# Performance work log

Measured on AMD Instinct MI355X. Metric: run time of the kernel, lower is better.

The kernel has to match this reference:

```python
import jax, jax.numpy as jnp
import numpy as np

N_NODES = 100000
N_EDGES = 3200000
N_HID = 3
HEAD_OUT = 1024


def setup_inputs() -> dict:
    key = jax.random.key(0)
    ks = jax.random.split(key, 8)
    feat1 = jax.random.normal(ks[0], (N_NODES, 1), dtype=jnp.float32)
    feat2 = jax.random.normal(ks[1], (N_NODES, 1), dtype=jnp.float32)
    norm = jax.random.uniform(ks[2], (N_EDGES,), dtype=jnp.float32)
    src = jax.random.randint(ks[3], (N_EDGES,), 0, N_NODES, dtype=jnp.int32)
    dst = jax.random.randint(ks[4], (N_EDGES,), 0, N_NODES, dtype=jnp.int32)
    # per-layer GIN apply_func Linear(1,1): weight [n_hid,1,1], bias [n_hid,1]
    gin_w = jax.random.normal(ks[5], (N_HID, 1, 1), dtype=jnp.float32)
    gin_b = jax.random.normal(ks[6], (N_HID, 1), dtype=jnp.float32) * 0.1
    # head Linear(num_nodes, 1024), stored as [in, out]
    net_w = jax.random.normal(ks[7], (N_NODES, HEAD_OUT), dtype=jnp.float32) * (1.0 / np.sqrt(N_NODES))
    net_b = jnp.zeros((HEAD_OUT,), dtype=jnp.float32)
    return {"feat1": feat1, "feat2": feat2, "norm": norm, "src": src, "dst": dst,
            "gin_w": gin_w, "gin_b": gin_b, "net_w": net_w, "net_b": net_b}


def reference(feat1, feat2, norm, src, dst, gin_w, gin_b, net_w, net_b):
    n = feat1.shape[0]
    e_dtype = feat1.dtype
    # in-degree (same every layer); DGL mean over mailbox divides by in-degree
    deg = jax.ops.segment_sum(jnp.ones((src.shape[0],), e_dtype), dst, num_segments=n)
    inv_deg = (1.0 / jnp.maximum(deg, 1.0))[:, None]  # [N,1]

    def forward_each(feat):
        x = feat  # [N,1]
        saved = []
        for l in range(gin_w.shape[0]):
            msg = x[src] * norm[:, None]                                # gather + edge weight [E,1]
            agg = jax.ops.segment_sum(msg, dst, num_segments=n) * inv_deg  # mean aggregate [N,1]
            rst = (x + agg) @ gin_w[l].T + gin_b[l]                     # GIN: (1+eps)*x + agg, eps=0, then Linear
            saved.append(rst)                                           # forward hook captures pre-relu output
            x = jax.nn.relu(rst)
        feats = jnp.mean(jnp.stack(saved), axis=0)  # mean over layers [N,1]
        h = feats.reshape(1, -1)                    # flatten -> [1, N]
        return h @ net_w + net_b                    # [1, 1024]

    x1 = forward_each(feat1)
    x2 = forward_each(feat2)
    return jax.nn.sigmoid(jnp.sum(x1 * x2, axis=1, keepdims=True))  # [1,1]
```

## Files before the change

kernel.cpp:

```cpp
#include <hip/hip_runtime.h>
#include <math.h>

static constexpr int NN  = 100000;
static constexpr int NE  = 3200000;
static constexpr int HO  = 1024;
static constexpr int BSH = 5;
static constexpr int BMASK = 31;
static constexpr int NB  = 3125;
static constexpr int NBP = NB + 1;
static constexpr int PB  = 256;
static constexpr int AT  = 1024;
static constexpr int CHUNK = NE / PB;
static constexpr int PER_A = (NB + AT - 1) / AT;
static constexpr int RPB = 50;
static constexpr int HB  = NN / RPB;
static constexpr int CAP = 2048;
static constexpr int BT  = 49;
static constexpr int BSTRIDE = 1536;

typedef float f4v __attribute__((ext_vector_type(4)));

__device__ __forceinline__ int bucket_swz(int blk) {
    int x = blk & 7, g = blk >> 3;
    return (x < 5) ? x * 391 + g : 1955 + (x - 5) * 390 + g;
}

__global__ __launch_bounds__(AT) void partA_k(const float* __restrict__ f1,
                                              const float* __restrict__ f2,
                                              const int* __restrict__ src,
                                              const int* __restrict__ dst,
                                              const float* __restrict__ norm,
                                              int* __restrict__ loffg,
                                              uint2* __restrict__ blocked,
                                              float2* __restrict__ x0,
                                              float* __restrict__ xacc) {
    __shared__ int hist[NB];
    __shared__ int wt[16];
    int blk = blockIdx.x, t = threadIdx.x;
    int lane = t & 63, w = t >> 6;
    int gi = blk * AT + t;
    if (gi < NN) x0[gi] = make_float2(f1[gi], f2[gi]);
    if (blk == 0) {
        for (int i = t; i < 2 * HO; i += AT) xacc[i] = 0.f;
    }
    for (int i = t; i < NB; i += AT) hist[i] = 0;
    __syncthreads();
    int base = blk * CHUNK;
    for (int i = t; i < CHUNK; i += AT)
        atomicAdd(&hist[dst[base + i] >> BSH], 1);
    __syncthreads();
    int loc[PER_A]; int s = 0;
    int b0 = t * PER_A;
#pragma unroll
    for (int k = 0; k < PER_A; ++k) {
        int i = b0 + k;
        int v = (i < NB) ? hist[i] : 0;
        loc[k] = s; s += v;
    }
    int incl = s;
#pragma unroll
    for (int off = 1; off < 64; off <<= 1) {
        int v = __shfl_up(incl, off, 64);
        if (lane >= off) incl += v;
    }
    if (lane == 63) wt[w] = incl;
    __syncthreads();
    int wpre = 0;
#pragma unroll
    for (int k = 0; k < 16; ++k) if (k < w) wpre += wt[k];
    int carry = wpre + incl - s;
#pragma unroll
    for (int k = 0; k < PER_A; ++k) {
        int i = b0 + k;
        if (i < NB) {
            int e = carry + loc[k];
            loffg[blk * NBP + i] = e;
            hist[i] = e;
        }
    }
    __syncthreads();
    for (int i = t; i < CHUNK; i += AT) {
        int e = base + i;
        int d = dst[e];
        int pos = atomicAdd(&hist[d >> BSH], 1);
        blocked[base + pos] = make_uint2((unsigned)src[e] | ((unsigned)(d & BMASK) << 17),
                                         __float_as_uint(norm[e]));
    }
}

__global__ __launch_bounds__(256) void transT_k(const int* __restrict__ loffg,
                                                int* __restrict__ loffT) {
    __shared__ int tile[64][65];
    int bx = blockIdx.x % BT;
    int ky = blockIdx.x / BT;
    int tx = threadIdx.x & 63, ty = threadIdx.x >> 6;
    int b = bx * 64 + tx;
#pragma unroll
    for (int j = 0; j < 16; ++j) {
        int k = ky * 64 + ty + j * 4;
        tile[ty + j * 4][tx] = (b < NB) ? loffg[k * NBP + b] : 0;
    }
    __syncthreads();
#pragma unroll
    for (int j = 0; j < 16; ++j) {
        int row = ty + j * 4;
        int bb = bx * 64 + row;
        if (bb < NB) loffT[(size_t)bb * PB + ky * 64 + tx] = tile[tx][row];
    }
}

__global__ __launch_bounds__(256) void sortB_k(const uint2* __restrict__ blocked,
                                               const int* __restrict__ loffT,
                                               unsigned* __restrict__ s2out,
                                               int2* __restrict__ noff) {
    __shared__ uint2 rec[CAP];
    __shared__ int wtot[4];
    __shared__ int cnt[32], curs[32];
    __shared__ float inv[32];
    int t = threadIdx.x;
    int lane = t & 63, w = t >> 6;
    int b = bucket_swz(blockIdx.x);
    int gbase = b * BSTRIDE;
    int o0 = loffT[(size_t)b * PB + t];
    int o1 = (b == NB - 1) ? CHUNK : loffT[(size_t)(b + 1) * PB + t];
    int len = o1 - o0;
    if (t < 32) cnt[t] = 0;
    int incl = len;
#pragma unroll
    for (int off = 1; off < 64; off <<= 1) {
        int v = __shfl_up(incl, off, 64);
        if (lane >= off) incl += v;
    }
    if (lane == 63) wtot[w] = incl;
    __syncthreads();
    int wpre = 0, total = 0;
#pragma unroll
    for (int k = 0; k < 4; ++k) {
        int tv = wtot[k];
        if (k < w) wpre += tv;
        total += tv;
    }
    int start = wpre + incl - len;
    if (total > CAP) total = CAP;
    {
        int lm = (len > 0) ? len - 1 : 0;
        int o0c = (o0 < CHUNK - 1) ? o0 : CHUNK - 1;
        const uint2* srcq = blocked + (size_t)t * CHUNK + o0c;
        uint2 q0 = srcq[0];
        uint2 q1 = srcq[lm < 1 ? lm : 1];
        uint2 q2 = srcq[lm < 2 ? lm : 2];
        uint2 q3 = srcq[lm < 3 ? lm : 3];
        uint2 q4 = srcq[lm < 4 ? lm : 4];
        uint2 q5 = srcq[lm < 5 ? lm : 5];
        uint2 q6 = srcq[lm < 6 ? lm : 6];
        uint2 q7 = srcq[lm < 7 ? lm : 7];
        if (len > 0 && start + 0 < CAP) rec[start + 0] = q0;
        if (len > 1 && start + 1 < CAP) rec[start + 1] = q1;
        if (len > 2 && start + 2 < CAP) rec[start + 2] = q2;
        if (len > 3 && start + 3 < CAP) rec[start + 3] = q3;
        if (len > 4 && start + 4 < CAP) rec[start + 4] = q4;
        if (len > 5 && start + 5 < CAP) rec[start + 5] = q5;
        if (len > 6 && start + 6 < CAP) rec[start + 6] = q6;
        if (len > 7 && start + 7 < CAP) rec[start + 7] = q7;
        for (int j = 8; j < len; ++j)
            if (start + j < CAP) rec[start + j] = srcq[j];
    }
    __syncthreads();
    for (int i = t; i < total; i += 256)
        atomicAdd(&cnt[(rec[i].x >> 17) & BMASK], 1);
    __syncthreads();
    if (t < 32) {
        int c = cnt[t];
        int c4 = (c + 3) & ~3;
        int ic4 = c4;
#pragma unroll
        for (int off = 1; off < 32; off <<= 1) {
            int v = __shfl_up(ic4, off, 32);
            if (t >= off) ic4 += v;
        }
        int pre4 = ic4 - c4;
        curs[t] = pre4;
        inv[t] = 1.0f / fmaxf((float)c, 1.0f);
        noff[(b << BSH) + t] = make_int2(gbase + pre4, gbase + pre4 + c4);
        for (int j = c; j < c4; ++j) s2out[gbase + pre4 + j] = 0u;
    }
    __syncthreads();
    for (int i = t; i < total; i += 256) {
        uint2 r = rec[i];
        int lo = (r.x >> 17) & BMASK;
        int pos = atomicAdd(&curs[lo], 1);
        float v = __uint_as_float(r.y) * inv[lo];
        int q = (int)(v * 32768.f + 0.5f);
        if (q > 32767) q = 32767;
        s2out[gbase + pos] = (r.x & 131071u) | ((unsigned)q << 17);
    }
}

template<int L0>
__global__ __launch_bounds__(256) void layer_k(const unsigned* __restrict__ s2,
                                               const int2* __restrict__ noff,
                                               const float2* __restrict__ xin,
                                               float2* __restrict__ xout,
                                               float2* __restrict__ ssum,
                                               const float* __restrict__ gw,
                                               const float* __restrict__ gb, int l) {
    int gid = blockIdx.x * 256 + threadIdx.x;
    int node = gid >> 3, r = gid & 7;
    if (node >= NN) return;
    int2 no = noff[node];
    int i0 = no.x, i1 = no.y;
    float ax = 0.f, ay = 0.f;
    const float qs = 1.0f / 32768.0f;
    for (int i = i0 + 4 * r; i < i1; i += 32) {
        uint4 q = *reinterpret_cast<const uint4*>(s2 + i);
        float2 xa = xin[q.x & 131071u]; float wa = (float)(q.x >> 17) * qs;
        float2 xb = xin[q.y & 131071u]; float wb = (float)(q.y >> 17) * qs;
        float2 xc = xin[q.z & 131071u]; float wc = (float)(q.z >> 17) * qs;
        float2 xd = xin[q.w & 131071u]; float wd = (float)(q.w >> 17) * qs;
        ax = fmaf(xa.x, wa, ax); ay = fmaf(xa.y, wa, ay);
        ax = fmaf(xb.x, wb, ax); ay = fmaf(xb.y, wb, ay);
        ax = fmaf(xc.x, wc, ax); ay = fmaf(xc.y, wc, ay);
        ax = fmaf(xd.x, wd, ax); ay = fmaf(xd.y, wd, ay);
    }
#pragma unroll
    for (int off = 1; off < 8; off <<= 1) {
        ax += __shfl_xor(ax, off, 64);
        ay += __shfl_xor(ay, off, 64);
    }
    if (r == 0) {
        float wv = gw[l], bb = gb[l];
        float2 xv = xin[node];
        float rx = fmaf(xv.x + ax, wv, bb);
        float ry = fmaf(xv.y + ay, wv, bb);
        if (L0) ssum[node] = make_float2(rx, ry);
        else { float2 s = ssum[node]; ssum[node] = make_float2(s.x + rx, s.y + ry); }
        xout[node] = make_float2(fmaxf(rx, 0.f), fmaxf(ry, 0.f));
    }
}

__global__ __launch_bounds__(256) void head_k(const float2* __restrict__ ssum,
                                              const float* __restrict__ W,
                                              float* __restrict__ part) {
    __shared__ float sf0[RPB], sf1[RPB];
    int r0 = blockIdx.x * RPB;
    int t = threadIdx.x;
    const float sc = 1.0f / 3.0f;
    if (t < RPB) {
        float2 s = ssum[r0 + t];
        sf0[t] = s.x * sc;
        sf1[t] = s.y * sc;
    }
    __syncthreads();
    float ax1=0.f, ay1=0.f, az1=0.f, aw1=0.f;
    float ax2=0.f, ay2=0.f, az2=0.f, aw2=0.f;
    int j0 = t * 4;
    const f4v* Wp = reinterpret_cast<const f4v*>(W + (size_t)r0 * HO + j0);
#pragma unroll 5
    for (int k = 0; k < RPB; ++k) {
        f4v w4 = __builtin_nontemporal_load(Wp);
        Wp += HO / 4;
        float v1 = sf0[k], v2 = sf1[k];
        ax1 = fmaf(v1, w4.x, ax1); ay1 = fmaf(v1, w4.y, ay1);
        az1 = fmaf(v1, w4.z, az1); aw1 = fmaf(v1, w4.w, aw1);
        ax2 = fmaf(v2, w4.x, ax2); ay2 = fmaf(v2, w4.y, ay2);
        az2 = fmaf(v2, w4.z, az2); aw2 = fmaf(v2, w4.w, aw2);
    }
    float* pp = part + (size_t)blockIdx.x * 2048;
    pp[j0]   = ax1; pp[j0+1] = ay1; pp[j0+2] = az1; pp[j0+3] = aw1;
    pp[1024+j0]   = ax2; pp[1024+j0+1] = ay2;
    pp[1024+j0+2] = az2; pp[1024+j0+3] = aw2;
}

__global__ __launch_bounds__(256) void reduce_k(const float* __restrict__ part,
                                                float* __restrict__ xacc) {
    int gid = blockIdx.x * 256 + threadIdx.x;
    int j = gid & 2047;
    int seg = gid >> 11;
    int b0 = (seg * HB) >> 5, b1 = ((seg + 1) * HB) >> 5;
    float s = 0.f;
    for (int b = b0; b < b1; ++b) s += part[(size_t)b * 2048 + j];
    atomicAdd(&xacc[j], s);
}

__global__ void final_k(const float* __restrict__ xacc, const float* __restrict__ nb,
                        float* __restrict__ out) {
    __shared__ float red[256];
    int t = threadIdx.x;
    float v = 0.f;
    for (int j = t; j < HO; j += 256)
        v += (xacc[j] + nb[j]) * (xacc[HO + j] + nb[j]);
    red[t] = v;
    __syncthreads();
    for (int s = 128; s > 0; s >>= 1) {
        if (t < s) red[t] += red[t + s];
        __syncthreads();
    }
    if (t == 0) out[0] = 1.0f / (1.0f + expf(-red[0]));
}

extern "C" void kernel_launch(void* const* d_in, const int* in_sizes, int n_in,
                              void* d_out, int out_size, void* d_ws, size_t ws_size,
                              hipStream_t stream) {
    const float* feat1 = (const float*)d_in[0];
    const float* feat2 = (const float*)d_in[1];
    const float* norm  = (const float*)d_in[2];
    const int*   src   = (const int*)  d_in[3];
    const int*   dst   = (const int*)  d_in[4];
    const float* gin_w = (const float*)d_in[5];
    const float* gin_b = (const float*)d_in[6];
    const float* net_w = (const float*)d_in[7];
    const float* net_b = (const float*)d_in[8];
    float* out = (float*)d_out;

    char* p = (char*)d_ws;
    uint2* blocked   = (uint2*)p;             p += (size_t)NE * 8;
    float* part      = (float*)blocked;
    unsigned* sorted2 = (unsigned*)p;         p += (size_t)NB * BSTRIDE * 4;
    int*   loffg     = (int*)p;               p += (size_t)PB * NBP * 4;
    int*   loffT     = (int*)p;               p += (size_t)NB * PB * 4;
    int2*  noff      = (int2*)p;              p += (size_t)NN * 8;
    float2* x0       = (float2*)p;            p += (size_t)NN * 8;
    float2* x1       = (float2*)p;            p += (size_t)NN * 8;
    float2* ssum     = (float2*)p;            p += (size_t)NN * 8;
    float* xacc      = (float*)p;             p += (size_t)2 * HO * 4;

    int lg = (NN * 8 + 255) / 256;

    partA_k<<<PB, AT, 0, stream>>>(feat1, feat2, src, dst, norm, loffg, blocked,
                                   x0, xacc);
    transT_k<<<BT * 4, 256, 0, stream>>>(loffg, loffT);
    sortB_k<<<NB, 256, 0, stream>>>(blocked, loffT, sorted2, noff);

    layer_k<1><<<lg, 256, 0, stream>>>(sorted2, noff, x0, x1, ssum, gin_w, gin_b, 0);
    layer_k<0><<<lg, 256, 0, stream>>>(sorted2, noff, x1, x0, ssum, gin_w, gin_b, 1);
    layer_k<0><<<lg, 256, 0, stream>>>(sorted2, noff, x0, x1, ssum, gin_w, gin_b, 2);

    head_k<<<HB, 256, 0, stream>>>(ssum, net_w, part);
    reduce_k<<<256, 256, 0, stream>>>(part, xacc);
    final_k<<<1, 256, 0, stream>>>(xacc, net_b, out);
}
```

Before: 215.7 us.

## Scatter edges directly into per-bucket global slots instead of chunk-local blocks

Replaces the chunk-local counting sort plus offset transpose with a separate histogram pass, a global-position scan kernel, and a scatter kernel that writes each edge into a fixed-size per-bucket slot. The bucket sort stage then reads each bucket contiguously instead of gathering from 256 small chunk segments. This adds an extra pass over dst and one more launch, and relies on buckets not exceeding the slot capacity.

```diff
diff --git a/kernel.cpp b/kernel.cpp
--- a/kernel.cpp
+++ b/kernel.cpp
@@ -7,16 +7,16 @@
 static constexpr int BSH = 5;
 static constexpr int BMASK = 31;
 static constexpr int NB  = 3125;
-static constexpr int NBP = NB + 1;
+static constexpr int CST = 3136;
 static constexpr int PB  = 256;
 static constexpr int AT  = 1024;
 static constexpr int CHUNK = NE / PB;
-static constexpr int PER_A = (NB + AT - 1) / AT;
 static constexpr int RPB = 50;
 static constexpr int HB  = NN / RPB;
-static constexpr int CAP = 2048;
-static constexpr int BT  = 49;
+static constexpr int SLOT = 2048;
+static constexpr int CAP  = 2048;
 static constexpr int BSTRIDE = 1536;
+static constexpr int BT2 = 49;
 
 typedef float f4v __attribute__((ext_vector_type(4)));
 
@@ -25,152 +25,108 @@
     return (x < 5) ? x * 391 + g : 1955 + (x - 5) * 390 + g;
 }
 
-__global__ __launch_bounds__(AT) void partA_k(const float* __restrict__ f1,
+__global__ __launch_bounds__(AT) void histA_k(const float* __restrict__ f1,
                                               const float* __restrict__ f2,
-                                              const int* __restrict__ src,
                                               const int* __restrict__ dst,
-                                              const float* __restrict__ norm,
-                                              int* __restrict__ loffg,
-                                              uint2* __restrict__ blocked,
+                                              int* __restrict__ cnt,
                                               float2* __restrict__ x0,
                                               float* __restrict__ xacc) {
     __shared__ int hist[NB];
-    __shared__ int wt[16];
     int blk = blockIdx.x, t = threadIdx.x;
-    int lane = t & 63, w = t >> 6;
     int gi = blk * AT + t;
     if (gi < NN) x0[gi] = make_float2(f1[gi], f2[gi]);
-    if (blk == 0) {
-        for (int i = t; i < 2 * HO; i += AT) xacc[i] = 0.f;
-    }
+    if (blk == 0 && t < 2 * HO) xacc[t] = 0.f;
     for (int i = t; i < NB; i += AT) hist[i] = 0;
     __syncthreads();
     int base = blk * CHUNK;
     for (int i = t; i < CHUNK; i += AT)
         atomicAdd(&hist[dst[base + i] >> BSH], 1);
     __syncthreads();
-    int loc[PER_A]; int s = 0;
-    int b0 = t * PER_A;
-#pragma unroll
-    for (int k = 0; k < PER_A; ++k) {
-        int i = b0 + k;
-        int v = (i < NB) ? hist[i] : 0;
-        loc[k] = s; s += v;
-    }
-    int incl = s;
-#pragma unroll
-    for (int off = 1; off < 64; off <<= 1) {
-        int v = __shfl_up(incl, off, 64);
-        if (lane >= off) incl += v;
-    }
-    if (lane == 63) wt[w] = incl;
-    __syncthreads();
-    int wpre = 0;
-#pragma unroll
-    for (int k = 0; k < 16; ++k) if (k < w) wpre += wt[k];
-    int carry = wpre + incl - s;
-#pragma unroll
-    for (int k = 0; k < PER_A; ++k) {
-        int i = b0 + k;
-        if (i < NB) {
-            int e = carry + loc[k];
-            loffg[blk * NBP + i] = e;
-            hist[i] = e;
+    for (int i = t; i < NB; i += AT) cnt[blk * CST + i] = hist[i];
+}
+
+__global__ __launch_bounds__(256) void gpos_k(const int* __restrict__ cnt,
+                                              int* __restrict__ gposT,
+                                              int* __restrict__ btot) {
+    __shared__ int tile[64][64];
+    __shared__ int sgsum[64][4];
+    __shared__ int carry[64];
+    int t = threadIdx.x;
+    int bl = t & 63, sg = t >> 6;
+    int b0 = blockIdx.x * 64;
+    if (sg == 0) carry[bl] = 0;
+    __syncthreads();
+    for (int kt = 0; kt < 4; ++kt) {
+        for (int idx = t; idx < 4096; idx += 256) {
+            int kl = idx >> 6, bb = idx & 63;
+            int b = b0 + bb;
+            tile[kl][bb] = (b < NB) ? cnt[(kt * 64 + kl) * CST + b] : 0;
         }
-    }
-    __syncthreads();
+        __syncthreads();
+        int s = 0;
+#pragma unroll
+        for (int j = 0; j < 16; ++j) s += tile[sg * 16 + j][bl];
+        sgsum[bl][sg] = s;
+        __syncthreads();
+        int base = carry[bl];
+        for (int g = 0; g < sg; ++g) base += sgsum[bl][g];
+        int b = b0 + bl;
+        if (b < NB) {
+            int run = base;
+#pragma unroll
+            for (int j = 0; j < 16; ++j) {
+                int k = kt * 64 + sg * 16 + j;
+                gposT[k * CST + b] = b * SLOT + run;
+                run += tile[sg * 16 + j][bl];
+            }
+        }
+        __syncthreads();
+        if (sg == 0) carry[bl] += sgsum[bl][0] + sgsum[bl][1] + sgsum[bl][2] + sgsum[bl][3];
+        __syncthreads();
+    }
+    if (sg == 0 && b0 + bl < NB) btot[b0 + bl] = carry[bl];
+}
+
+__global__ __launch_bounds__(AT) void scat_k(const int* __restrict__ src,
+                                             const int* __restrict__ dst,
+                                             const float* __restrict__ norm,
+                                             const int* __restrict__ gposT,
+                                             uint2* __restrict__ blocked2) {
+    __shared__ int cur[NB];
+    int blk = blockIdx.x, t = threadIdx.x;
+    for (int i = t; i < NB; i += AT) cur[i] = gposT[blk * CST + i];
+    __syncthreads();
+    int base = blk * CHUNK;
     for (int i = t; i < CHUNK; i += AT) {
         int e = base + i;
         int d = dst[e];
-        int pos = atomicAdd(&hist[d >> BSH], 1);
-        blocked[base + pos] = make_uint2((unsigned)src[e] | ((unsigned)(d & BMASK) << 17),
-                                         __float_as_uint(norm[e]));
-    }
-}
-
-__global__ __launch_bounds__(256) void transT_k(const int* __restrict__ loffg,
-                                                int* __restrict__ loffT) {
-    __shared__ int tile[64][65];
-    int bx = blockIdx.x % BT;
-    int ky = blockIdx.x / BT;
-    int tx = threadIdx.x & 63, ty = threadIdx.x >> 6;
-    int b = bx * 64 + tx;
-#pragma unroll
-    for (int j = 0; j < 16; ++j) {
-        int k = ky * 64 + ty + j * 4;
-        tile[ty + j * 4][tx] = (b < NB) ? loffg[k * NBP + b] : 0;
-    }
-    __syncthreads();
-#pragma unroll
-    for (int j = 0; j < 16; ++j) {
-        int row = ty + j * 4;
-        int bb = bx * 64 + row;
-        if (bb < NB) loffT[(size_t)bb * PB + ky * 64 + tx] = tile[tx][row];
-    }
-}
-
-__global__ __launch_bounds__(256) void sortB_k(const uint2* __restrict__ blocked,
-                                               const int* __restrict__ loffT,
+        int pos = atomicAdd(&cur[d >> BSH], 1);
+        blocked2[pos] = make_uint2((unsigned)src[e] | ((unsigned)(d & BMASK) << 17),
+                                   __float_as_uint(norm[e]));
+    }
+}
+
+__global__ __launch_bounds__(256) void sortB_k(const uint2* __restrict__ blocked2,
+                                               const int* __restrict__ btot,
                                                unsigned* __restrict__ s2out,
                                                int2* __restrict__ noff) {
     __shared__ uint2 rec[CAP];
-    __shared__ int wtot[4];
-    __shared__ int cnt[32], curs[32];
+    __shared__ int cnt32[32], curs[32];
     __shared__ float inv[32];
     int t = threadIdx.x;
-    int lane = t & 63, w = t >> 6;
     int b = bucket_swz(blockIdx.x);
     int gbase = b * BSTRIDE;
-    int o0 = loffT[(size_t)b * PB + t];
-    int o1 = (b == NB - 1) ? CHUNK : loffT[(size_t)(b + 1) * PB + t];
-    int len = o1 - o0;
-    if (t < 32) cnt[t] = 0;
-    int incl = len;
-#pragma unroll
-    for (int off = 1; off < 64; off <<= 1) {
-        int v = __shfl_up(incl, off, 64);
-        if (lane >= off) incl += v;
-    }
-    if (lane == 63) wtot[w] = incl;
-    __syncthreads();
-    int wpre = 0, total = 0;
-#pragma unroll
-    for (int k = 0; k < 4; ++k) {
-        int tv = wtot[k];
-        if (k < w) wpre += tv;
-        total += tv;
-    }
-    int start = wpre + incl - len;
+    int total = btot[b];
     if (total > CAP) total = CAP;
-    {
-        int lm = (len > 0) ? len - 1 : 0;
-        int o0c = (o0 < CHUNK - 1) ? o0 : CHUNK - 1;
-        const uint2* srcq = blocked + (size_t)t * CHUNK + o0c;
-        uint2 q0 = srcq[0];
-        uint2 q1 = srcq[lm < 1 ? lm : 1];
-        uint2 q2 = srcq[lm < 2 ? lm : 2];
-        uint2 q3 = srcq[lm < 3 ? lm : 3];
-        uint2 q4 = srcq[lm < 4 ? lm : 4];
-        uint2 q5 = srcq[lm < 5 ? lm : 5];
-        uint2 q6 = srcq[lm < 6 ? lm : 6];
-        uint2 q7 = srcq[lm < 7 ? lm : 7];
-        if (len > 0 && start + 0 < CAP) rec[start + 0] = q0;
-        if (len > 1 && start + 1 < CAP) rec[start + 1] = q1;
-        if (len > 2 && start + 2 < CAP) rec[start + 2] = q2;
-        if (len > 3 && start + 3 < CAP) rec[start + 3] = q3;
-        if (len > 4 && start + 4 < CAP) rec[start + 4] = q4;
-        if (len > 5 && start + 5 < CAP) rec[start + 5] = q5;
-        if (len > 6 && start + 6 < CAP) rec[start + 6] = q6;
-        if (len > 7 && start + 7 < CAP) rec[start + 7] = q7;
-        for (int j = 8; j < len; ++j)
-            if (start + j < CAP) rec[start + j] = srcq[j];
-    }
+    const uint2* sp = blocked2 + (size_t)b * SLOT;
+    if (t < 32) cnt32[t] = 0;
+    for (int i = t; i < total; i += 256) rec[i] = sp[i];
     __syncthreads();
     for (int i = t; i < total; i += 256)
-        atomicAdd(&cnt[(rec[i].x >> 17) & BMASK], 1);
+        atomicAdd(&cnt32[(rec[i].x >> 17) & BMASK], 1);
     __syncthreads();
     if (t < 32) {
-        int c = cnt[t];
+        int c = cnt32[t];
         int c4 = (c + 3) & ~3;
         int ic4 = c4;
 #pragma unroll
@@ -313,11 +269,12 @@
     float* out = (float*)d_out;
 
     char* p = (char*)d_ws;
-    uint2* blocked   = (uint2*)p;             p += (size_t)NE * 8;
-    float* part      = (float*)blocked;
+    uint2* blocked2  = (uint2*)p;             p += (size_t)NB * SLOT * 8;
+    float* part      = (float*)blocked2;
     unsigned* sorted2 = (unsigned*)p;         p += (size_t)NB * BSTRIDE * 4;
-    int*   loffg     = (int*)p;               p += (size_t)PB * NBP * 4;
-    int*   loffT     = (int*)p;               p += (size_t)NB * PB * 4;
+    int*   cnt       = (int*)p;               p += (size_t)PB * CST * 4;
+    int*   gposT     = (int*)p;               p += (size_t)PB * CST * 4;
+    int*   btot      = (int*)p;               p += ((size_t)NB * 4 + 15) & ~15ull;
     int2*  noff      = (int2*)p;              p += (size_t)NN * 8;
     float2* x0       = (float2*)p;            p += (size_t)NN * 8;
     float2* x1       = (float2*)p;            p += (size_t)NN * 8;
@@ -326,10 +283,10 @@
 
     int lg = (NN * 8 + 255) / 256;
 
-    partA_k<<<PB, AT, 0, stream>>>(feat1, feat2, src, dst, norm, loffg, blocked,
-                                   x0, xacc);
-    transT_k<<<BT * 4, 256, 0, stream>>>(loffg, loffT);
-    sortB_k<<<NB, 256, 0, stream>>>(blocked, loffT, sorted2, noff);
+    histA_k<<<PB, AT, 0, stream>>>(feat1, feat2, dst, cnt, x0, xacc);
+    gpos_k<<<BT2, 256, 0, stream>>>(cnt, gposT, btot);
+    scat_k<<<PB, AT, 0, stream>>>(src, dst, norm, gposT, blocked2);
+    sortB_k<<<NB, 256, 0, stream>>>(blocked2, btot, sorted2, noff);
 
     layer_k<1><<<lg, 256, 0, stream>>>(sorted2, noff, x0, x1, ssum, gin_w, gin_b, 0);
     layer_k<0><<<lg, 256, 0, stream>>>(sorted2, noff, x1, x0, ssum, gin_w, gin_b, 1);
```

After: 235.3 us. +9.1%, slower.
